# Performance work log

Measured on AMD Instinct MI355X. Metric: run time of the kernel, lower is better.

## Reference

```python
import jax, jax.numpy as jnp
import numpy as np

# Omelyan 4th-order symplectic coefficients
XI = 0.1786178958448091
LAM = -0.2123418310626054
CHI = -0.0662645826698185
C1, C2 = XI, CHI
C3 = 1.0 - 2.0 * (CHI + XI)
C4, C5 = CHI, XI
D1 = (1.0 - 2.0 * LAM) / 2.0
D2 = D3 = LAM
D4 = (1.0 - 2.0 * LAM) / 2.0

DT = 0.01
DT_SCALE = 1.0
PLASTICITY = 0.1
SING_THRESH = 1.0
SING_STRENGTH = 1.0

B, DIM, RANK = 4096, 1024, 256


def setup_inputs() -> dict:
    key = jax.random.key(0)
    ks = jax.random.split(key, 6)
    x = jax.random.normal(ks[0], (B, DIM), dtype=jnp.float32)
    v = jax.random.normal(ks[1], (B, DIM), dtype=jnp.float32)
    force = jax.random.normal(ks[2], (B, DIM), dtype=jnp.float32)
    # low-rank bilinear Christoffel factors, scaled for stability
    U = jax.random.normal(ks[3], (DIM, RANK), dtype=jnp.float32) * (1.0 / np.sqrt(DIM))
    W = jax.random.normal(ks[4], (RANK, DIM), dtype=jnp.float32) * (1.0 / np.sqrt(RANK))
    V_w = jax.random.normal(ks[5], (DIM,), dtype=jnp.float32)
    return {"x": x, "v": v, "force": force, "U": U, "W": W, "V_w": V_w, "steps": 4}


def _christoffel(tv, tx, U, W, V_w):
    # low-rank bilinear Gamma(v,v): project, square, expand
    h = tv @ U                      # [B, R]
    gamma = (h * h) @ W             # [B, D]
    # plasticity modulation (elementwise gate on position)
    gate = 1.0 + PLASTICITY * jnp.tanh(tx * V_w)
    # singularity amplification near origin
    r2 = jnp.sum(tx * tx, axis=-1, keepdims=True)
    sing = 1.0 + SING_STRENGTH * jnp.exp(-r2 / SING_THRESH)
    return gamma * gate * sing


def reference(x, v, force, U, W, V_w, steps):
    dt = DT * DT_SCALE

    def accel(tx, tv):
        return -_christoffel(tv, tx, U, W, V_w) + force

    curr_x, curr_v = x, v
    for _ in range(steps):
        x1 = curr_x + C1 * dt * curr_v
        v1 = curr_v + D1 * dt * accel(x1, curr_v)
        x2 = x1 + C2 * dt * v1
        v2 = v1 + D2 * dt * accel(x2, v1)
        x3 = x2 + C3 * dt * v2
        v3 = v2 + D3 * dt * accel(x3, v2)
        x4 = x3 + C4 * dt * v3
        v4 = v3 + D4 * dt * accel(x4, v3)
        curr_x = x4 + C5 * dt * v4
        curr_v = v4
    return (curr_x, curr_v)
```

## Files before the change

### kernel.cpp

```cpp
#include <hip/hip_runtime.h>
#include <math.h>

typedef short  bf16x8 __attribute__((ext_vector_type(8)));
typedef float  f32x4  __attribute__((ext_vector_type(4)));
typedef float  f32x2  __attribute__((ext_vector_type(2)));

#define DIM   1024
#define RANK  256
#define NROWS 16
#define NT    512
#define NWAVE 8
#define TOTAL_ROWS 4096
#define OUT_HALF (TOTAL_ROWS*DIM)

#define VS_OFF    0
#define H2_OFF    32768
#define XS_OFF    40960
#define WS_OFF    106496
#define SG_OFF    107008
#define SMEM_BYTES 107072

static constexpr double XI  = 0.1786178958448091;
static constexpr double LAM = -0.2123418310626054;
static constexpr double CHI = -0.0662645826698185;

__device__ __forceinline__ unsigned short f2bf(float f) {
    unsigned u = __builtin_bit_cast(unsigned, f);
    u += 0x7FFFu + ((u >> 16) & 1u);
    return (unsigned short)(u >> 16);
}
__device__ __forceinline__ float bf2f(unsigned short b) {
    return __builtin_bit_cast(float, ((unsigned)b) << 16);
}

__device__ __forceinline__ int vs_addr(int m, int kb) {
    return VS_OFF + ((m * 2048 + kb) ^ ((m & 7) << 4));
}
__device__ __forceinline__ int h2_addr(int m, int kb) {
    return H2_OFF + ((m * 512 + kb) ^ ((m & 7) << 4));
}

__global__ __launch_bounds__(256)
void prep_pack(const float* __restrict__ U, const float* __restrict__ Wm,
               bf16x8* __restrict__ pk)
{
    const int tid  = blockIdx.x * 256 + threadIdx.x;
    const int lane = tid & 63;
    const int frag = tid >> 6;
    bf16x8 o;
    if (frag < 512) {
        const int kt = frag >> 4, nt = frag & 15;
        const int krow = kt * 32 + (lane >> 4) * 8;
        const int n    = nt * 16 + (lane & 15);
        #pragma unroll
        for (int j = 0; j < 8; ++j) o[j] = (short)f2bf(U[(krow + j) * RANK + n]);
    } else {
        const int f = frag - 512;
        const int kt = f >> 6, nt = f & 63;
        const int krow = kt * 32 + (lane >> 4) * 8;
        const int n    = nt * 16 + (lane & 15);
        #pragma unroll
        for (int j = 0; j < 8; ++j) o[j] = (short)f2bf(Wm[(krow + j) * DIM + n]);
    }
    pk[frag * 64 + lane] = o;
}

__global__ __launch_bounds__(NT)
void omelyan_mfma(const float* __restrict__ x_in,
                  const float* __restrict__ v_in,
                  const float* __restrict__ force,
                  const float* __restrict__ Vw,
                  const int* __restrict__ steps_p,
                  const bf16x8* __restrict__ pk,
                  float* __restrict__ out)
{
    extern __shared__ char smem[];
    float* wsums = (float*)(smem + WS_OFF);
    float* sings = (float*)(smem + SG_OFF);
    float* xsp   = (float*)(smem + XS_OFF);

    const int t    = threadIdx.x;
    const int lane = t & 63;
    const int w    = t >> 6;
    const int row0 = blockIdx.x * NROWS;
    const int nsteps = steps_p[0];

    const float dt = 0.01f;

    float vr[NROWS][2];
    const f32x2 vw = *(const f32x2*)&Vw[2 * t];

    #pragma unroll
    for (int m = 0; m < NROWS; ++m) {
        const int base = (row0 + m) * DIM + 2 * t;
        const f32x2 xv = *(const f32x2*)&x_in[base];
        const f32x2 vv = *(const f32x2*)&v_in[base];
        vr[m][0] = vv[0]; vr[m][1] = vv[1];
        *(f32x2*)&xsp[m * 1024 + 2 * t] = xv;
        const unsigned p = (unsigned)f2bf(vv[0]) | ((unsigned)f2bf(vv[1]) << 16);
        *(unsigned*)(smem + vs_addr(m, 4 * t)) = p;
    }
    __syncthreads();

    #pragma unroll 1
    for (int step = 0; step < nsteps; ++step) {
        #pragma unroll 1
        for (int sub = 0; sub < 4; ++sub) {
            const float cdt = dt * (sub == 0 ? (float)XI :
                                    sub == 1 ? (float)CHI :
                                    sub == 2 ? (float)(1.0 - 2.0 * (CHI + XI)) :
                                               (float)CHI);
            const float ddt = dt * ((sub == 0 || sub == 3)
                                    ? (float)((1.0 - 2.0 * LAM) * 0.5)
                                    : (float)LAM);

            #pragma unroll
            for (int m = 0; m < NROWS; ++m) {
                f32x2 x2 = *(f32x2*)&xsp[m * 1024 + 2 * t];
                x2[0] = fmaf(cdt, vr[m][0], x2[0]);
                x2[1] = fmaf(cdt, vr[m][1], x2[1]);
                *(f32x2*)&xsp[m * 1024 + 2 * t] = x2;
                float s = fmaf(x2[0], x2[0], x2[1] * x2[1]);
                #pragma unroll
                for (int off = 32; off >= 1; off >>= 1) s += __shfl_xor(s, off, 64);
                if (lane == 0) wsums[m * NWAVE + w] = s;
            }
            __syncthreads();
            if (t < NROWS) {
                float r2 = 0.f;
                #pragma unroll
                for (int q = 0; q < NWAVE; ++q) r2 += wsums[t * NWAVE + q];
                sings[t] = 1.f + exp2f(-r2 * 1.4426950408889634f);
            }

            {
                f32x4 h0 = {0.f,0.f,0.f,0.f}, h1 = {0.f,0.f,0.f,0.f};
                bf16x8 bb[4][2];
                #pragma unroll
                for (int d = 0; d < 4; ++d) {
                    bb[d][0] = pk[(d * 16 + 2 * w + 0) * 64 + lane];
                    bb[d][1] = pk[(d * 16 + 2 * w + 1) * 64 + lane];
                }
                #pragma unroll 4
                for (int ks = 0; ks < 32; ++ks) {
                    const bf16x8 a = *(const bf16x8*)(smem + vs_addr(lane & 15, ks * 64 + (lane >> 4) * 16));
                    h0 = __builtin_amdgcn_mfma_f32_16x16x32_bf16(a, bb[ks & 3][0], h0, 0, 0, 0);
                    h1 = __builtin_amdgcn_mfma_f32_16x16x32_bf16(a, bb[ks & 3][1], h1, 0, 0, 0);
                    if (ks + 4 < 32) {
                        bb[ks & 3][0] = pk[((ks + 4) * 16 + 2 * w + 0) * 64 + lane];
                        bb[ks & 3][1] = pk[((ks + 4) * 16 + 2 * w + 1) * 64 + lane];
                    }
                }
                #pragma unroll
                for (int r = 0; r < 4; ++r) {
                    const int m = (lane >> 4) * 4 + r;
                    const int c = lane & 15;
                    *(unsigned short*)(smem + h2_addr(m, 2 * ((2 * w + 0) * 16 + c))) = f2bf(h0[r] * h0[r]);
                    *(unsigned short*)(smem + h2_addr(m, 2 * ((2 * w + 1) * 16 + c))) = f2bf(h1[r] * h1[r]);
                }
            }
            __syncthreads();

            {
                f32x4 g0 = {0.f,0.f,0.f,0.f}, g1 = {0.f,0.f,0.f,0.f};
                bf16x8 bb[4][2];
                #pragma unroll
                for (int d = 0; d < 4; ++d) {
                    bb[d][0] = pk[512 * 64 + (d * 64 + 0 * 16 + 2 * w + 0) * 64 + lane];
                    bb[d][1] = pk[512 * 64 + (d * 64 + 0 * 16 + 2 * w + 1) * 64 + lane];
                }
                #pragma unroll 4
                for (int u = 0; u < 32; ++u) {
                    const int kk = u & 7;
                    const int pass = u >> 3;
                    const bf16x8 a = *(const bf16x8*)(smem + h2_addr(lane & 15, kk * 64 + (lane >> 4) * 16));
                    g0 = __builtin_amdgcn_mfma_f32_16x16x32_bf16(a, bb[u & 3][0], g0, 0, 0, 0);
                    g1 = __builtin_amdgcn_mfma_f32_16x16x32_bf16(a, bb[u & 3][1], g1, 0, 0, 0);
                    if (u + 4 < 32) {
                        const int u2 = u + 4;
                        const int kk2 = u2 & 7, p2 = u2 >> 3;
                        bb[u & 3][0] = pk[512 * 64 + (kk2 * 64 + p2 * 16 + 2 * w + 0) * 64 + lane];
                        bb[u & 3][1] = pk[512 * 64 + (kk2 * 64 + p2 * 16 + 2 * w + 1) * 64 + lane];
                    }
                    if (kk == 7) {
                        #pragma unroll
                        for (int r = 0; r < 4; ++r) {
                            const int m = (lane >> 4) * 4 + r;
                            const int c = lane & 15;
                            *(unsigned short*)(smem + vs_addr(m, 2 * ((pass * 16 + 2 * w + 0) * 16 + c))) = f2bf(g0[r]);
                            *(unsigned short*)(smem + vs_addr(m, 2 * ((pass * 16 + 2 * w + 1) * 16 + c))) = f2bf(g1[r]);
                        }
                        g0 = (f32x4){0.f,0.f,0.f,0.f};
                        g1 = (f32x4){0.f,0.f,0.f,0.f};
                    }
                }
            }
            __syncthreads();

            #pragma unroll
            for (int m = 0; m < NROWS; ++m) {
                const f32x2 fm = *(const f32x2*)&force[(row0 + m) * DIM + 2 * t];
                const f32x2 x2 = *(const f32x2*)&xsp[m * 1024 + 2 * t];
                const unsigned gu = *(const unsigned*)(smem + vs_addr(m, 4 * t));
                const float gL = bf2f((unsigned short)(gu & 0xFFFFu));
                const float gH = bf2f((unsigned short)(gu >> 16));
                const float sing = sings[m];
                unsigned pp = 0;
                #pragma unroll
                for (int j = 0; j < 2; ++j) {
                    const float g  = j ? gH : gL;
                    const float z  = x2[j] * vw[j];
                    const float e  = exp2f(z * 2.885390081777927f);
                    const float th = 1.f - 2.f / (e + 1.f);
                    const float gate = fmaf(0.1f, th, 1.f);
                    const float a = fm[j] - g * gate * sing;
                    vr[m][j] = fmaf(ddt, a, vr[m][j]);
                    pp |= ((unsigned)f2bf(vr[m][j])) << (16 * j);
                }
                *(unsigned*)(smem + vs_addr(m, 4 * t)) = pp;
            }
        }

        const float c5dt = dt * (float)XI;
        #pragma unroll
        for (int m = 0; m < NROWS; ++m) {
            f32x2 x2 = *(f32x2*)&xsp[m * 1024 + 2 * t];
            x2[0] = fmaf(c5dt, vr[m][0], x2[0]);
            x2[1] = fmaf(c5dt, vr[m][1], x2[1]);
            *(f32x2*)&xsp[m * 1024 + 2 * t] = x2;
        }
    }

    __syncthreads();

    #pragma unroll
    for (int m = 0; m < NROWS; ++m) {
        const int base = (row0 + m) * DIM + 2 * t;
        const f32x2 x2 = *(const f32x2*)&xsp[m * 1024 + 2 * t];
        f32x2 vo; vo[0] = vr[m][0]; vo[1] = vr[m][1];
        *(f32x2*)&out[base] = x2;
        *(f32x2*)&out[OUT_HALF + base] = vo;
    }
}

extern "C" void kernel_launch(void* const* d_in, const int* in_sizes, int n_in,
                              void* d_out, int out_size, void* d_ws, size_t ws_size,
                              hipStream_t stream) {
    const float* x_in  = (const float*)d_in[0];
    const float* v_in  = (const float*)d_in[1];
    const float* force = (const float*)d_in[2];
    const float* Umat  = (const float*)d_in[3];
    const float* Wmat  = (const float*)d_in[4];
    const float* Vw    = (const float*)d_in[5];
    const int*   steps = (const int*)d_in[6];
    float* out = (float*)d_out;
    bf16x8* pk = (bf16x8*)d_ws;

    (void)hipFuncSetAttribute((const void*)omelyan_mfma,
                              hipFuncAttributeMaxDynamicSharedMemorySize,
                              SMEM_BYTES);

    prep_pack<<<dim3(256), dim3(256), 0, stream>>>(Umat, Wmat, pk);
    omelyan_mfma<<<dim3(TOTAL_ROWS / NROWS), dim3(NT), SMEM_BYTES, stream>>>(
        x_in, v_in, force, Vw, steps, pk, out);
}
```

Baseline: 275.2 us.

## Switch Christoffel low-rank matmuls from bf16 to fp8 e4m3 MFMA

Both low-rank GEMMs (v@U and h^2@W) now run on fp8 e4m3 MFMA instead of bf16. The packed weights, the velocity tile and the squared projections are quantized to e4m3 with fixed scale factors, and the gamma output is also stored as e4m3 and decoded by software before the update. This halves the weight bytes streamed from global memory and the LDS footprint, and fp8 MFMA is faster. In exchange it adds software conversion cost and heavy precision loss, with a risk of overflow or saturation in the fixed scaling that may break tolerance.

```diff
diff --git a/kernel.cpp b/kernel.cpp
--- a/kernel.cpp
+++ b/kernel.cpp
@@ -1,7 +1,6 @@
 #include <hip/hip_runtime.h>
 #include <math.h>
 
-typedef short  bf16x8 __attribute__((ext_vector_type(8)));
 typedef float  f32x4  __attribute__((ext_vector_type(4)));
 typedef float  f32x2  __attribute__((ext_vector_type(2)));
 
@@ -14,55 +13,75 @@
 #define OUT_HALF (TOTAL_ROWS*DIM)
 
 #define VS_OFF    0
-#define H2_OFF    32768
-#define XS_OFF    40960
-#define WS_OFF    106496
-#define SG_OFF    107008
-#define SMEM_BYTES 107072
+#define H2_OFF    16384
+#define XS_OFF    20480
+#define WS_OFF    86016
+#define SG_OFF    86528
+#define SMEM_BYTES 86592
 
 static constexpr double XI  = 0.1786178958448091;
 static constexpr double LAM = -0.2123418310626054;
 static constexpr double CHI = -0.0662645826698185;
+
+__device__ __forceinline__ unsigned f2e4m3(float f) {
+    unsigned u = __builtin_bit_cast(unsigned, f);
+    const unsigned s = (u >> 24) & 0x80u;
+    unsigned a = u & 0x7FFFFFFFu;
+    const float af = __builtin_bit_cast(float, a);
+    if (af < 0.015625f) {
+        return s | (unsigned)(int)rintf(af * 512.0f);
+    }
+    a += 0x7FFFFu + ((a >> 20) & 1u);
+    if (a > 0x43E00000u) return s | 0x7Eu;
+    const unsigned e = (a >> 23) & 0xFFu;
+    return s | ((e - 120u) << 3) | ((a >> 20) & 7u);
+}
+__device__ __forceinline__ float e4m32f(unsigned b) {
+    const unsigned e = (b >> 3) & 0xFu, m = b & 7u;
+    const float mag = (e != 0)
+        ? __builtin_bit_cast(float, ((e + 120u) << 23) | (m << 20))
+        : (float)m * 0.001953125f;
+    return (b & 0x80u) ? -mag : mag;
+}
 
 __device__ __forceinline__ unsigned short f2bf(float f) {
     unsigned u = __builtin_bit_cast(unsigned, f);
     u += 0x7FFFu + ((u >> 16) & 1u);
     return (unsigned short)(u >> 16);
 }
-__device__ __forceinline__ float bf2f(unsigned short b) {
-    return __builtin_bit_cast(float, ((unsigned)b) << 16);
-}
-
-__device__ __forceinline__ int vs_addr(int m, int kb) {
-    return VS_OFF + ((m * 2048 + kb) ^ ((m & 7) << 4));
-}
-__device__ __forceinline__ int h2_addr(int m, int kb) {
-    return H2_OFF + ((m * 512 + kb) ^ ((m & 7) << 4));
+
+__device__ __forceinline__ int vs_addr(int m, int k) {
+    return VS_OFF + ((m * 1024 + k) ^ ((m & 7) << 3));
+}
+__device__ __forceinline__ int h2_addr(int m, int k) {
+    return H2_OFF + ((m * 256 + k) ^ ((m & 7) << 3));
 }
 
 __global__ __launch_bounds__(256)
 void prep_pack(const float* __restrict__ U, const float* __restrict__ Wm,
-               bf16x8* __restrict__ pk)
+               long* __restrict__ pk8)
 {
     const int tid  = blockIdx.x * 256 + threadIdx.x;
     const int lane = tid & 63;
     const int frag = tid >> 6;
-    bf16x8 o;
+    unsigned long long o = 0;
     if (frag < 512) {
         const int kt = frag >> 4, nt = frag & 15;
         const int krow = kt * 32 + (lane >> 4) * 8;
         const int n    = nt * 16 + (lane & 15);
         #pragma unroll
-        for (int j = 0; j < 8; ++j) o[j] = (short)f2bf(U[(krow + j) * RANK + n]);
+        for (int j = 0; j < 8; ++j)
+            o |= (unsigned long long)f2e4m3(8.0f * U[(krow + j) * RANK + n]) << (8 * j);
     } else {
         const int f = frag - 512;
         const int kt = f >> 6, nt = f & 63;
         const int krow = kt * 32 + (lane >> 4) * 8;
         const int n    = nt * 16 + (lane & 15);
         #pragma unroll
-        for (int j = 0; j < 8; ++j) o[j] = (short)f2bf(Wm[(krow + j) * DIM + n]);
-    }
-    pk[frag * 64 + lane] = o;
+        for (int j = 0; j < 8; ++j)
+            o |= (unsigned long long)f2e4m3(8.0f * Wm[(krow + j) * DIM + n]) << (8 * j);
+    }
+    pk8[frag * 64 + lane] = (long)o;
 }
 
 __global__ __launch_bounds__(NT)
@@ -71,7 +90,7 @@
                   const float* __restrict__ force,
                   const float* __restrict__ Vw,
                   const int* __restrict__ steps_p,
-                  const bf16x8* __restrict__ pk,
+                  const long* __restrict__ pk8,
                   float* __restrict__ out)
 {
     extern __shared__ char smem[];
@@ -97,8 +116,8 @@
         const f32x2 vv = *(const f32x2*)&v_in[base];
         vr[m][0] = vv[0]; vr[m][1] = vv[1];
         *(f32x2*)&xsp[m * 1024 + 2 * t] = xv;
-        const unsigned p = (unsigned)f2bf(vv[0]) | ((unsigned)f2bf(vv[1]) << 16);
-        *(unsigned*)(smem + vs_addr(m, 4 * t)) = p;
+        const unsigned short p = (unsigned short)(f2e4m3(vv[0]) | (f2e4m3(vv[1]) << 8));
+        *(unsigned short*)(smem + vs_addr(m, 2 * t)) = p;
     }
     __syncthreads();
 
@@ -135,60 +154,64 @@
 
             {
                 f32x4 h0 = {0.f,0.f,0.f,0.f}, h1 = {0.f,0.f,0.f,0.f};
-                bf16x8 bb[4][2];
+                long bb[4][2];
                 #pragma unroll
                 for (int d = 0; d < 4; ++d) {
-                    bb[d][0] = pk[(d * 16 + 2 * w + 0) * 64 + lane];
-                    bb[d][1] = pk[(d * 16 + 2 * w + 1) * 64 + lane];
+                    bb[d][0] = pk8[(d * 16 + 2 * w + 0) * 64 + lane];
+                    bb[d][1] = pk8[(d * 16 + 2 * w + 1) * 64 + lane];
                 }
                 #pragma unroll 4
                 for (int ks = 0; ks < 32; ++ks) {
-                    const bf16x8 a = *(const bf16x8*)(smem + vs_addr(lane & 15, ks * 64 + (lane >> 4) * 16));
-                    h0 = __builtin_amdgcn_mfma_f32_16x16x32_bf16(a, bb[ks & 3][0], h0, 0, 0, 0);
-                    h1 = __builtin_amdgcn_mfma_f32_16x16x32_bf16(a, bb[ks & 3][1], h1, 0, 0, 0);
+                    const long a = *(const long*)(smem + vs_addr(lane & 15, ks * 32 + (lane >> 4) * 8));
+                    h0 = __builtin_amdgcn_mfma_f32_16x16x32_fp8_fp8(a, bb[ks & 3][0], h0, 0, 0, 0);
+                    h1 = __builtin_amdgcn_mfma_f32_16x16x32_fp8_fp8(a, bb[ks & 3][1], h1, 0, 0, 0);
                     if (ks + 4 < 32) {
-                        bb[ks & 3][0] = pk[((ks + 4) * 16 + 2 * w + 0) * 64 + lane];
-                        bb[ks & 3][1] = pk[((ks + 4) * 16 + 2 * w + 1) * 64 + lane];
+                        bb[ks & 3][0] = pk8[((ks + 4) * 16 + 2 * w + 0) * 64 + lane];
+                        bb[ks & 3][1] = pk8[((ks + 4) * 16 + 2 * w + 1) * 64 + lane];
                     }
                 }
                 #pragma unroll
                 for (int r = 0; r < 4; ++r) {
                     const int m = (lane >> 4) * 4 + r;
                     const int c = lane & 15;
-                    *(unsigned short*)(smem + h2_addr(m, 2 * ((2 * w + 0) * 16 + c))) = f2bf(h0[r] * h0[r]);
-                    *(unsigned short*)(smem + h2_addr(m, 2 * ((2 * w + 1) * 16 + c))) = f2bf(h1[r] * h1[r]);
+                    *(unsigned char*)(smem + h2_addr(m, (2 * w + 0) * 16 + c)) =
+                        (unsigned char)f2e4m3(h0[r] * h0[r] * 0.25f);
+                    *(unsigned char*)(smem + h2_addr(m, (2 * w + 1) * 16 + c)) =
+                        (unsigned char)f2e4m3(h1[r] * h1[r] * 0.25f);
                 }
             }
             __syncthreads();
 
             {
                 f32x4 g0 = {0.f,0.f,0.f,0.f}, g1 = {0.f,0.f,0.f,0.f};
-                bf16x8 bb[4][2];
+                long bb[4][2];
                 #pragma unroll
                 for (int d = 0; d < 4; ++d) {
-                    bb[d][0] = pk[512 * 64 + (d * 64 + 0 * 16 + 2 * w + 0) * 64 + lane];
-                    bb[d][1] = pk[512 * 64 + (d * 64 + 0 * 16 + 2 * w + 1) * 64 + lane];
+                    bb[d][0] = pk8[512 * 64 + (d * 64 + 2 * w + 0) * 64 + lane];
+                    bb[d][1] = pk8[512 * 64 + (d * 64 + 2 * w + 1) * 64 + lane];
                 }
                 #pragma unroll 4
                 for (int u = 0; u < 32; ++u) {
                     const int kk = u & 7;
                     const int pass = u >> 3;
-                    const bf16x8 a = *(const bf16x8*)(smem + h2_addr(lane & 15, kk * 64 + (lane >> 4) * 16));
-                    g0 = __builtin_amdgcn_mfma_f32_16x16x32_bf16(a, bb[u & 3][0], g0, 0, 0, 0);
-                    g1 = __builtin_amdgcn_mfma_f32_16x16x32_bf16(a, bb[u & 3][1], g1, 0, 0, 0);
+                    const long a = *(const long*)(smem + h2_addr(lane & 15, kk * 32 + (lane >> 4) * 8));
+                    g0 = __builtin_amdgcn_mfma_f32_16x16x32_fp8_fp8(a, bb[u & 3][0], g0, 0, 0, 0);
+                    g1 = __builtin_amdgcn_mfma_f32_16x16x32_fp8_fp8(a, bb[u & 3][1], g1, 0, 0, 0);
                     if (u + 4 < 32) {
                         const int u2 = u + 4;
                         const int kk2 = u2 & 7, p2 = u2 >> 3;
-                        bb[u & 3][0] = pk[512 * 64 + (kk2 * 64 + p2 * 16 + 2 * w + 0) * 64 + lane];
-                        bb[u & 3][1] = pk[512 * 64 + (kk2 * 64 + p2 * 16 + 2 * w + 1) * 64 + lane];
+                        bb[u & 3][0] = pk8[512 * 64 + (kk2 * 64 + p2 * 16 + 2 * w + 0) * 64 + lane];
+                        bb[u & 3][1] = pk8[512 * 64 + (kk2 * 64 + p2 * 16 + 2 * w + 1) * 64 + lane];
                     }
                     if (kk == 7) {
                         #pragma unroll
                         for (int r = 0; r < 4; ++r) {
                             const int m = (lane >> 4) * 4 + r;
                             const int c = lane & 15;
-                            *(unsigned short*)(smem + vs_addr(m, 2 * ((pass * 16 + 2 * w + 0) * 16 + c))) = f2bf(g0[r]);
-                            *(unsigned short*)(smem + vs_addr(m, 2 * ((pass * 16 + 2 * w + 1) * 16 + c))) = f2bf(g1[r]);
+                            *(unsigned char*)(smem + vs_addr(m, (pass * 16 + 2 * w + 0) * 16 + c)) =
+                                (unsigned char)f2e4m3(g0[r] * 0.0078125f);
+                            *(unsigned char*)(smem + vs_addr(m, (pass * 16 + 2 * w + 1) * 16 + c)) =
+                                (unsigned char)f2e4m3(g1[r] * 0.0078125f);
                         }
                         g0 = (f32x4){0.f,0.f,0.f,0.f};
                         g1 = (f32x4){0.f,0.f,0.f,0.f};
@@ -201,9 +224,9 @@
             for (int m = 0; m < NROWS; ++m) {
                 const f32x2 fm = *(const f32x2*)&force[(row0 + m) * DIM + 2 * t];
                 const f32x2 x2 = *(const f32x2*)&xsp[m * 1024 + 2 * t];
-                const unsigned gu = *(const unsigned*)(smem + vs_addr(m, 4 * t));
-                const float gL = bf2f((unsigned short)(gu & 0xFFFFu));
-                const float gH = bf2f((unsigned short)(gu >> 16));
+                const unsigned gu = *(const unsigned short*)(smem + vs_addr(m, 2 * t));
+                const float gL = e4m32f(gu & 0xFFu);
+                const float gH = e4m32f((gu >> 8) & 0xFFu);
                 const float sing = sings[m];
                 unsigned pp = 0;
                 #pragma unroll
@@ -215,9 +238,9 @@
                     const float gate = fmaf(0.1f, th, 1.f);
                     const float a = fm[j] - g * gate * sing;
                     vr[m][j] = fmaf(ddt, a, vr[m][j]);
-                    pp |= ((unsigned)f2bf(vr[m][j])) << (16 * j);
-                }
-                *(unsigned*)(smem + vs_addr(m, 4 * t)) = pp;
+                    pp |= f2e4m3(vr[m][j]) << (8 * j);
+                }
+                *(unsigned short*)(smem + vs_addr(m, 2 * t)) = (unsigned short)pp;
             }
         }
 
@@ -254,13 +277,13 @@
     const float* Vw    = (const float*)d_in[5];
     const int*   steps = (const int*)d_in[6];
     float* out = (float*)d_out;
-    bf16x8* pk = (bf16x8*)d_ws;
+    long* pk8 = (long*)d_ws;
 
     (void)hipFuncSetAttribute((const void*)omelyan_mfma,
                               hipFuncAttributeMaxDynamicSharedMemorySize,
                               SMEM_BYTES);
 
-    prep_pack<<<dim3(256), dim3(256), 0, stream>>>(Umat, Wmat, pk);
+    prep_pack<<<dim3(256), dim3(256), 0, stream>>>(Umat, Wmat, pk8);
     omelyan_mfma<<<dim3(TOTAL_ROWS / NROWS), dim3(NT), SMEM_BYTES, stream>>>(
-        x_in, v_in, force, Vw, steps, pk, out);
-}
+        x_in, v_in, force, Vw, steps, pk8, out);
+}
```

After: 350.6 us. 27.4% more time.
